# Kernel tuning notes

Hardware: AMD Instinct MI355X
Metric: run time of the kernel (lower is better)

## Reference

```python
import jax, jax.numpy as jnp
import numpy as np

B, S, D = 8, 1024, 256
H = 8            # num_heads
HD = D // H      # head_dim
FF = 1024        # expert hidden_dim
E = 8            # num_experts
K = 2            # top-k
L = 2            # num_layers
OUT = 1000       # output_dim
EPS = 1e-5


def setup_inputs() -> dict:
    key = jax.random.key(0)
    ks = jax.random.split(key, 20)
    std = 0.02
    inp = {
        "x": jax.random.normal(ks[0], (B, S, D), jnp.float32),
        "qkv_w": jax.random.normal(ks[1], (L, D, 3 * D), jnp.float32) * std,
        "qkv_b": jnp.zeros((L, 3 * D), jnp.float32),
        "attn_w": jax.random.normal(ks[2], (L, D, D), jnp.float32) * std,
        "attn_b": jnp.zeros((L, D), jnp.float32),
        "gate_w": jax.random.normal(ks[3], (L, D, E), jnp.float32) * std,
        "gate_b": jnp.zeros((L, E), jnp.float32),
        "e_w1": jax.random.normal(ks[4], (L, E, D, FF), jnp.float32) * std,
        "e_b1": jnp.zeros((L, E, FF), jnp.float32),
        "e_w2": jax.random.normal(ks[5], (L, E, FF, D), jnp.float32) * std,
        "e_b2": jnp.zeros((L, E, D), jnp.float32),
        "ln1_g": jnp.ones((D,), jnp.float32),
        "ln1_b": jnp.zeros((D,), jnp.float32),
        "ln2_g": jnp.ones((D,), jnp.float32),
        "ln2_b": jnp.zeros((D,), jnp.float32),
        "head_w": jax.random.normal(ks[6], (D, OUT), jnp.float32) * std,
        "head_b": jnp.zeros((OUT,), jnp.float32),
    }
    return inp


def _layer_norm(x, g, b):
    m = jnp.mean(x, -1, keepdims=True)
    v = jnp.mean((x - m) ** 2, -1, keepdims=True)
    return (x - m) / jnp.sqrt(v + EPS) * g + b


def _attention(x, w_qkv, b_qkv, w_o, b_o):
    # x: [B,S,D]
    qkv = (x @ w_qkv + b_qkv).reshape(B, S, 3, H, HD)
    q, k, v = jnp.moveaxis(qkv, 2, 0)            # each [B,S,H,HD]
    q = q.transpose(0, 2, 1, 3)                   # [B,H,S,HD]
    k = k.transpose(0, 2, 1, 3)
    v = v.transpose(0, 2, 1, 3)
    attn = jax.nn.softmax(jnp.einsum('bhqd,bhkd->bhqk', q, k) * (HD ** -0.5), axis=-1)
    o = jnp.einsum('bhqk,bhkd->bhqd', attn, v).transpose(0, 2, 1, 3).reshape(B, S, D)
    return o @ w_o + b_o


def _moe(x, gw, gb, w1, b1, w2, b2):
    # x: [B,S,D] -> tokens [T,D]
    xf = x.reshape(-1, D)
    gates = xf @ gw + gb                           # [T,E]
    scores, idx = jax.lax.top_k(gates, K)          # [T,K]
    gate_w = jax.nn.softmax(scores, axis=-1)       # [T,K]
    # dense all-expert compute, then gather selected experts per token
    h = jax.nn.gelu(jnp.einsum('td,edh->teh', xf, w1) + b1, approximate=False)
    eo = jnp.einsum('teh,ehd->ted', h, w2) + b2    # [T,E,D]
    sel = jnp.take_along_axis(eo, idx[:, :, None], axis=1)  # [T,K,D]
    out = jnp.sum(gate_w[:, :, None] * sel, axis=1)
    return out.reshape(B, S, D)


def reference(x, qkv_w, qkv_b, attn_w, attn_b, gate_w, gate_b,
              e_w1, e_b1, e_w2, e_b2, ln1_g, ln1_b, ln2_g, ln2_b,
              head_w, head_b):
    for l in range(L):
        x = x + _attention(_layer_norm(x, ln1_g, ln1_b),
                           qkv_w[l], qkv_b[l], attn_w[l], attn_b[l])
        x = x + _moe(_layer_norm(x, ln2_g, ln2_b),
                     gate_w[l], gate_b[l], e_w1[l], e_b1[l], e_w2[l], e_b2[l])
    pooled = jnp.mean(x, axis=1)                   # [B,D]
    return pooled @ head_w + head_b                # [B,OUT]
```

## Files before the change

kernel.cpp:

```cpp
#include <hip/hip_runtime.h>
#include <math.h>

#define TOK   8192
#define DIM   256
#define NH    8
#define HDIM  32
#define FFD   1024
#define NE    8
#define NL    2
#define NOUT  1000
#define NSLOT 16384

typedef unsigned int uint;
typedef unsigned short ushort;
typedef __attribute__((ext_vector_type(8))) short short8;
typedef __attribute__((ext_vector_type(4))) float f32x4;

#define WS_X     ((size_t)0)
#define WS_LN    (WS_X    + (size_t)TOK*DIM)
#define WS_QKV   (WS_LN   + (size_t)TOK*DIM)
#define WS_H     (WS_QKV  + (size_t)TOK*3*DIM)
#define WS_SOUT  (WS_H    + (size_t)NSLOT*256)
#define WS_GV    (WS_SOUT + (size_t)NSLOT*256)
#define WS_PP    (WS_GV   + (size_t)TOK*2)
#define WS_POOL  (WS_PP   + (size_t)8*32*256)
#define WS_INT   (WS_POOL + (size_t)8*256)
#define WS_U16   (WS_INT  + (size_t)54144)
#define WS_BIG   (WS_U16  + (size_t)2359296)

#define IB_COUNTS   0
#define IB_NTILES   8
#define IB_OFFS     16
#define IB_CURS     24
#define IB_TILE_E   32
#define IB_TILE_R0  320
#define IB_TILE_RE  608
#define IB_GIDX     896
#define IB_SPOS     17280
#define IB_STOK     33664
#define IB_BLKC     50048
#define IB_BLKB     52096

__device__ __forceinline__ float gelu_exact(float v) {
    return 0.5f * v * (1.0f + erff(v * 0.70710678118654752f));
}

__device__ __forceinline__ ushort rnd_bf16(float x) {
    uint u = __float_as_uint(x);
    return (ushort)((u + 0x7FFFu + ((u >> 16) & 1u)) >> 16);
}

__device__ __forceinline__ void split2(float x, ushort& h, ushort& lo) {
    uint u = __float_as_uint(x);
    uint hh = (u + 0x7FFFu + ((u >> 16) & 1u)) >> 16;
    h = (ushort)hh;
    float hf = __uint_as_float(hh << 16);
    float l = x - hf;
    uint ul = __float_as_uint(l);
    lo = (ushort)((ul + 0x7FFFu + ((ul >> 16) & 1u)) >> 16);
}

__device__ __forceinline__ void gld16(const ushort* g, ushort* l) {
    __builtin_amdgcn_global_load_lds(
        (const __attribute__((address_space(1))) uint*)g,
        (__attribute__((address_space(3))) uint*)l, 16, 0, 0);
}

template<bool WF32>
__global__ __launch_bounds__(256) void ln_split(const float* __restrict__ x,
                                                float* __restrict__ out,
                                                ushort* __restrict__ ohi,
                                                const float* __restrict__ g,
                                                const float* __restrict__ b) {
    int wave = threadIdx.x >> 6;
    int lane = threadIdx.x & 63;
    int t = blockIdx.x * 4 + wave;
    const float* xp = x + (size_t)t * DIM;
    float4 v = *(const float4*)&xp[lane * 4];
    float s = v.x + v.y + v.z + v.w;
    #pragma unroll
    for (int off = 32; off; off >>= 1) s += __shfl_xor(s, off);
    float mean = s * (1.0f / 256.0f);
    float dx = v.x - mean, dy = v.y - mean, dz = v.z - mean, dw = v.w - mean;
    float vs = dx * dx + dy * dy + dz * dz + dw * dw;
    #pragma unroll
    for (int off = 32; off; off >>= 1) vs += __shfl_xor(vs, off);
    float inv = rsqrtf(vs * (1.0f / 256.0f) + 1e-5f);
    float4 gg = *(const float4*)&g[lane * 4];
    float4 bb = *(const float4*)&b[lane * 4];
    float o0 = dx * inv * gg.x + bb.x;
    float o1 = dy * inv * gg.y + bb.y;
    float o2 = dz * inv * gg.z + bb.z;
    float o3 = dw * inv * gg.w + bb.w;
    size_t idx = (size_t)t * DIM + lane * 4;
    if (WF32) {
        float4 o; o.x = o0; o.y = o1; o.z = o2; o.w = o3;
        *(float4*)&out[idx] = o;
    }
    uint2 ph;
    ph.x = (uint)rnd_bf16(o0) | ((uint)rnd_bf16(o1) << 16);
    ph.y = (uint)rnd_bf16(o2) | ((uint)rnd_bf16(o3) << 16);
    *(uint2*)&ohi[idx] = ph;
}

template<bool WLO>
__global__ __launch_bounds__(256) void split_transpose(const float* __restrict__ src,
                                                       ushort* __restrict__ dhi,
                                                       ushort* __restrict__ dlo,
                                                       int K, int N) {
    int z = blockIdx.z;
    const float* s = src + (size_t)z * K * N;
    ushort* th = dhi + (size_t)z * K * N;
    ushort* tl = dlo + (size_t)z * K * N;
    __shared__ float tile[32][33];
    int k0 = blockIdx.x * 32, n0 = blockIdx.y * 32;
    int tx = threadIdx.x & 31, ty = threadIdx.x >> 5;
    #pragma unroll
    for (int i = 0; i < 4; ++i) {
        int k = k0 + ty + i * 8;
        tile[ty + i * 8][tx] = s[(size_t)k * N + n0 + tx];
    }
    __syncthreads();
    #pragma unroll
    for (int i = 0; i < 4; ++i) {
        int n = n0 + ty + i * 8;
        float v = tile[tx][ty + i * 8];
        ushort h, lo;
        split2(v, h, lo);
        th[(size_t)n * K + k0 + tx] = h;
        if (WLO) tl[(size_t)n * K + k0 + tx] = lo;
    }
}


template<int MODE, int APASS>
__global__ __launch_bounds__(256) void mfma_dense128x64(const ushort* __restrict__ Ah,
                                                        const ushort* __restrict__ Al,
                                                        const ushort* __restrict__ Bh,
                                                        const ushort* __restrict__ Bl,
                                                        const float* __restrict__ bias,
                                                        float* __restrict__ C,
                                                        ushort* __restrict__ Chi, int N) {
    __shared__ ushort LAh[128][32], LBh[64][32], LBl[64][32];
    __shared__ ushort LAl[APASS == 2 ? 128 : 2][32];
    int tid = threadIdx.x;
    int w = tid >> 6, l = tid & 63, c = l & 15, G = l >> 4;
    int row0 = blockIdx.x * 128, col0 = blockIdx.y * 64;
    int lr = l >> 2, sd = l & 3;
    int rA0 = w * 16 + lr, rA1 = 64 + rA0;
    size_t ga0 = (size_t)(row0 + rA0) * 256 + ((sd ^ ((rA0 >> 1) & 3)) << 3);
    size_t ga1 = (size_t)(row0 + rA1) * 256 + ((sd ^ ((rA1 >> 1) & 3)) << 3);
    size_t gb0 = (size_t)(col0 + rA0) * 256 + ((sd ^ ((rA0 >> 1) & 3)) << 3);
    ushort* dA0h = &LAh[w * 16][0];      ushort* dA1h = &LAh[64 + w * 16][0];
    ushort* dBh  = &LBh[w * 16][0];      ushort* dBl  = &LBl[w * 16][0];
    f32x4 acc[2][4] = {};
    for (int k0 = 0; k0 < 256; k0 += 32) {
        gld16(&Ah[ga0 + k0], dA0h);
        gld16(&Ah[ga1 + k0], dA1h);
        if (APASS == 2) {
            gld16(&Al[ga0 + k0], &LAl[w * 16][0]);
            gld16(&Al[ga1 + k0], &LAl[64 + w * 16][0]);
        }
        gld16(&Bh[gb0 + k0], dBh);
        gld16(&Bl[gb0 + k0], dBl);
        __syncthreads();
        int ar = w * 32 + c;
        short8 a_h[2], a_l[2];
        #pragma unroll
        for (int i = 0; i < 2; ++i) {
            int r = ar + i * 16;
            int sg = (G ^ ((r >> 1) & 3)) << 3;
            a_h[i] = *(const short8*)&LAh[r][sg];
            if (APASS == 2) a_l[i] = *(const short8*)&LAl[r][sg];
        }
        #pragma unroll
        for (int j = 0; j < 4; ++j) {
            int r = j * 16 + c;
            int sg = (G ^ ((r >> 1) & 3)) << 3;
            short8 b_h = *(const short8*)&LBh[r][sg];
            short8 b_l = *(const short8*)&LBl[r][sg];
            #pragma unroll
            for (int i = 0; i < 2; ++i) {
                acc[i][j] = __builtin_amdgcn_mfma_f32_16x16x32_bf16(a_h[i], b_h, acc[i][j], 0, 0, 0);
                acc[i][j] = __builtin_amdgcn_mfma_f32_16x16x32_bf16(a_h[i], b_l, acc[i][j], 0, 0, 0);
                if (APASS == 2)
                    acc[i][j] = __builtin_amdgcn_mfma_f32_16x16x32_bf16(a_l[i], b_h, acc[i][j], 0, 0, 0);
            }
        }
        __syncthreads();
    }
    int rbase = row0 + w * 32 + G * 4;
    #pragma unroll
    for (int i = 0; i < 2; ++i) {
        #pragma unroll
        for (int j = 0; j < 4; ++j) {
            int gc = col0 + j * 16 + c;
            float bv = bias[gc];
            #pragma unroll
            for (int rr = 0; rr < 4; ++rr) {
                int grow = rbase + i * 16 + rr;
                size_t idx = (size_t)grow * N + gc;
                float v = acc[i][j][rr] + bv;
                if (MODE == 1) v += C[idx];
                if (MODE == 3) {
                    Chi[idx] = rnd_bf16(v);
                } else {
                    C[idx] = v;
                }
            }
        }
    }
}

__global__ __launch_bounds__(256) void vt_kernel(const ushort* __restrict__ qkvh,
                                                 ushort* __restrict__ vth) {
    int bh = blockIdx.y;
    int b = bh >> 3, h = bh & 7;
    int kv0 = blockIdx.x * 32;
    __shared__ ushort smh[32][33];
    int tid = threadIdx.x;
    #pragma unroll
    for (int p = 0; p < 4; ++p) {
        int kv = p * 8 + (tid >> 5);
        int d = tid & 31;
        size_t src = ((size_t)(b * 1024 + kv0 + kv)) * 768 + 512 + h * 32 + d;
        smh[kv][d] = qkvh[src];
    }
    __syncthreads();
    #pragma unroll
    for (int p = 0; p < 4; ++p) {
        int d = p * 8 + (tid >> 5);
        int kv = tid & 31;
        size_t dst = ((size_t)(bh * 32 + d)) * 1024 + kv0 + kv;
        vth[dst] = smh[kv][d];
    }
}

__global__ __launch_bounds__(256, 4) void attention_mfma(const ushort* __restrict__ qkvh,
                                                         const ushort* __restrict__ vth,
                                                         ushort* __restrict__ ohi) {
    int b = blockIdx.z, h = blockIdx.y;
    int q0 = blockIdx.x * 64;
    int tid = threadIdx.x;
    int w = tid >> 6, l = tid & 63;
    int c = l & 15, g = l >> 4;
    __shared__ ushort Kh[64][40];
    __shared__ ushort VTh[32][72];
    __shared__ ushort Ph[4][16][76];

    size_t qbase = ((size_t)(b * 1024 + q0 + w * 16 + c)) * 768 + h * 32 + g * 8;
    short8 qa_h = *(const short8*)&qkvh[qbase];

    f32x4 acc_o[2] = {};
    float lpart[4] = {0.f, 0.f, 0.f, 0.f};
    const float scale = 0.17677669529663687f;

    int sr = tid >> 2, sc8 = (tid & 3) * 8;
    size_t kgbase = ((size_t)(b * 1024 + sr)) * 768 + 256 + h * 32 + sc8;
    int vd = tid >> 3, vk8 = (tid & 7) * 8;
    size_t vtbase = ((size_t)((b * 8 + h) * 32 + vd)) * 1024 + vk8;

    for (int kv0 = 0; kv0 < 1024; kv0 += 64) {
        __syncthreads();
        *(uint4*)&Kh[sr][sc8]  = *(const uint4*)&qkvh[kgbase + (size_t)kv0 * 768];
        *(uint4*)&VTh[vd][vk8] = *(const uint4*)&vth[vtbase + kv0];
        __syncthreads();

        f32x4 s4[4];
        #pragma unroll
        for (int t = 0; t < 4; ++t) {
            short8 kh = *(const short8*)&Kh[t * 16 + c][g * 8];
            f32x4 a = {};
            a = __builtin_amdgcn_mfma_f32_16x16x32_bf16(qa_h, kh, a, 0, 0, 0);
            s4[t] = a;
        }

        #pragma unroll
        for (int rr = 0; rr < 4; ++rr) {
            float sum = 0.f;
            #pragma unroll
            for (int t = 0; t < 4; ++t) {
                float p = __expf(s4[t][rr] * scale);
                uint u = __float_as_uint(p);
                uint r = (u + 0x7FFFu + ((u >> 16) & 1u)) >> 16;
                Ph[w][g * 4 + rr][t * 16 + c] = (ushort)r;
                sum += __uint_as_float(r << 16);
            }
            lpart[rr] += sum;
        }
        asm volatile("s_waitcnt lgkmcnt(0)" ::: "memory");

        #pragma unroll
        for (int kt = 0; kt < 2; ++kt) {
            short8 pah = *(const short8*)&Ph[w][c][kt * 32 + g * 8];
            #pragma unroll
            for (int T = 0; T < 2; ++T) {
                short8 vh = *(const short8*)&VTh[T * 16 + c][kt * 32 + g * 8];
                acc_o[T] = __builtin_amdgcn_mfma_f32_16x16x32_bf16(pah, vh, acc_o[T], 0, 0, 0);
            }
        }
    }

    #pragma unroll
    for (int rr = 0; rr < 4; ++rr) {
        float s = lpart[rr];
        s += __shfl_xor(s, 1);
        s += __shfl_xor(s, 2);
        s += __shfl_xor(s, 4);
        s += __shfl_xor(s, 8);
        lpart[rr] = s;
    }

    #pragma unroll
    for (int rr = 0; rr < 4; ++rr) {
        float inv = 1.0f / lpart[rr];
        int q = q0 + w * 16 + g * 4 + rr;
        #pragma unroll
        for (int T = 0; T < 2; ++T) {
            float v = acc_o[T][rr] * inv;
            size_t idx = (size_t)(b * 1024 + q) * 256 + h * 32 + T * 16 + c;
            ohi[idx] = rnd_bf16(v);
        }
    }
}

__global__ __launch_bounds__(256) void mfma_ffn1_12864(const ushort* __restrict__ Ah,
                                                       const ushort* __restrict__ W1h,
                                                       const float* __restrict__ b1l,
                                                       ushort* __restrict__ hh,
                                                       const int* __restrict__ ib,
                                                       int c0, int hFF) {
    int tileIdx = blockIdx.x;
    if (tileIdx >= ib[IB_NTILES]) return;
    int e = ib[IB_TILE_E + tileIdx];
    int row0 = ib[IB_TILE_R0 + tileIdx];
    int rowend = ib[IB_TILE_RE + tileIdx];
    __shared__ ushort LAh[128][32], LBh[64][32];
    __shared__ int tok[128];
    int tid = threadIdx.x;
    if (tid < 128) {
        int sr = row0 + tid;
        tok[tid] = ib[IB_STOK + (sr < rowend ? sr : row0)];
    }
    __syncthreads();
    int w = tid >> 6, l = tid & 63, c = l & 15, G = l >> 4;
    int lr = l >> 2, sd = l & 3;
    int rA0 = w * 16 + lr, rA1 = 64 + rA0;
    int colbase = blockIdx.y * 64;
    const ushort* Bh = W1h + (size_t)e * 262144 + (size_t)(c0 + colbase) * 256;
    size_t ga0 = (size_t)tok[rA0] * 256 + ((sd ^ ((rA0 >> 1) & 3)) << 3);
    size_t ga1 = (size_t)tok[rA1] * 256 + ((sd ^ ((rA1 >> 1) & 3)) << 3);
    size_t gb0 = (size_t)rA0 * 256 + ((sd ^ ((rA0 >> 1) & 3)) << 3);
    ushort* dA0h = &LAh[w * 16][0];      ushort* dA1h = &LAh[64 + w * 16][0];
    ushort* dBh  = &LBh[w * 16][0];
    f32x4 acc[2][4] = {};
    for (int k0 = 0; k0 < 256; k0 += 32) {
        gld16(&Ah[ga0 + k0], dA0h);
        gld16(&Ah[ga1 + k0], dA1h);
        gld16(&Bh[gb0 + k0], dBh);
        __syncthreads();
        int ar = w * 32 + c;
        short8 a_h[2];
        #pragma unroll
        for (int i = 0; i < 2; ++i) {
            int r = ar + i * 16;
            int sg = (G ^ ((r >> 1) & 3)) << 3;
            a_h[i] = *(const short8*)&LAh[r][sg];
        }
        #pragma unroll
        for (int j = 0; j < 4; ++j) {
            int r = j * 16 + c;
            int sg = (G ^ ((r >> 1) & 3)) << 3;
            short8 b_h = *(const short8*)&LBh[r][sg];
            #pragma unroll
            for (int i = 0; i < 2; ++i) {
                acc[i][j] = __builtin_amdgcn_mfma_f32_16x16x32_bf16(a_h[i], b_h, acc[i][j], 0, 0, 0);
            }
        }
        __syncthreads();
    }
    int rbase = row0 + w * 32 + G * 4;
    #pragma unroll
    for (int i = 0; i < 2; ++i) {
        #pragma unroll
        for (int j = 0; j < 4; ++j) {
            int cl = colbase + j * 16 + c;
            float bv = b1l[(size_t)e * FFD + c0 + cl];
            #pragma unroll
            for (int rr = 0; rr < 4; ++rr) {
                int sr = rbase + i * 16 + rr;
                if (sr < rowend) {
                    float v = gelu_exact(acc[i][j][rr] + bv);
                    hh[(size_t)sr * hFF + cl] = rnd_bf16(v);
                }
            }
        }
    }
}

__global__ __launch_bounds__(256) void mfma_ffn2_12864(const ushort* __restrict__ Ah,
                                                       const ushort* __restrict__ W2h,
                                                       const float* __restrict__ b2l,
                                                       float* __restrict__ sout,
                                                       const int* __restrict__ ib,
                                                       int c0, int hFF) {
    int tileIdx = blockIdx.x;
    if (tileIdx >= ib[IB_NTILES]) return;
    int e = ib[IB_TILE_E + tileIdx];
    int row0 = ib[IB_TILE_R0 + tileIdx];
    int rowend = ib[IB_TILE_RE + tileIdx];
    __shared__ ushort LAh[128][32], LBh[64][32];
    int tid = threadIdx.x;
    int w = tid >> 6, l = tid & 63, c = l & 15, G = l >> 4;
    int lr = l >> 2, sd = l & 3;
    int rA0 = w * 16 + lr, rA1 = 64 + rA0;
    int colbase = blockIdx.y * 64;
    const ushort* Bh = W2h + (size_t)e * 262144;
    size_t ga0 = (size_t)(row0 + rA0) * hFF + ((sd ^ ((rA0 >> 1) & 3)) << 3);
    size_t ga1 = (size_t)(row0 + rA1) * hFF + ((sd ^ ((rA1 >> 1) & 3)) << 3);
    size_t gb0 = (size_t)(colbase + rA0) * 1024 + c0 + ((sd ^ ((rA0 >> 1) & 3)) << 3);
    ushort* dA0h = &LAh[w * 16][0];      ushort* dA1h = &LAh[64 + w * 16][0];
    ushort* dBh  = &LBh[w * 16][0];
    f32x4 acc[2][4] = {};
    for (int k0 = 0; k0 < hFF; k0 += 32) {
        gld16(&Ah[ga0 + k0], dA0h);
        gld16(&Ah[ga1 + k0], dA1h);
        gld16(&Bh[gb0 + k0], dBh);
        __syncthreads();
        int ar = w * 32 + c;
        short8 a_h[2];
        #pragma unroll
        for (int i = 0; i < 2; ++i) {
            int r = ar + i * 16;
            int sg = (G ^ ((r >> 1) & 3)) << 3;
            a_h[i] = *(const short8*)&LAh[r][sg];
        }
        #pragma unroll
        for (int j = 0; j < 4; ++j) {
            int r = j * 16 + c;
            int sg = (G ^ ((r >> 1) & 3)) << 3;
            short8 b_h = *(const short8*)&LBh[r][sg];
            #pragma unroll
            for (int i = 0; i < 2; ++i) {
                acc[i][j] = __builtin_amdgcn_mfma_f32_16x16x32_bf16(a_h[i], b_h, acc[i][j], 0, 0, 0);
            }
        }
        __syncthreads();
    }
    int rbase = row0 + w * 32 + G * 4;
    #pragma unroll
    for (int i = 0; i < 2; ++i) {
        #pragma unroll
        for (int j = 0; j < 4; ++j) {
            int n = colbase + j * 16 + c;
            float bv = b2l[(size_t)e * DIM + n];
            #pragma unroll
            for (int rr = 0; rr < 4; ++rr) {
                int sr = rbase + i * 16 + rr;
                if (sr < rowend) {
                    size_t idx = (size_t)sr * 256 + n;
                    if (c0 == 0) sout[idx] = acc[i][j][rr] + bv;
                    else         sout[idx] += acc[i][j][rr];
                }
            }
        }
    }
}

__global__ __launch_bounds__(256) void gate_topk(const float* __restrict__ lnb,
                                                 const float* __restrict__ gw,
                                                 const float* __restrict__ gb,
                                                 float* __restrict__ gv, int* __restrict__ ib) {
    __shared__ int hist[8];
    int tid = threadIdx.x;
    if (tid < 8) hist[tid] = 0;
    __syncthreads();
    int grp = tid >> 3, ln8 = tid & 7;
    int t = blockIdx.x * 32 + grp;
    const float* x = lnb + (size_t)t * DIM + ln8 * 32;
    const float* wb = gw + (size_t)ln8 * 32 * 8;
    float g[8] = {};
    #pragma unroll
    for (int d4 = 0; d4 < 8; ++d4) {
        float4 xv = *(const float4*)&x[d4 * 4];
        const float* wr = wb + d4 * 32;
        float4 wa0 = *(const float4*)&wr[0],  wb0 = *(const float4*)&wr[4];
        float4 wa1 = *(const float4*)&wr[8],  wb1 = *(const float4*)&wr[12];
        float4 wa2 = *(const float4*)&wr[16], wb2 = *(const float4*)&wr[20];
        float4 wa3 = *(const float4*)&wr[24], wb3 = *(const float4*)&wr[28];
        g[0] += xv.x * wa0.x + xv.y * wa1.x + xv.z * wa2.x + xv.w * wa3.x;
        g[1] += xv.x * wa0.y + xv.y * wa1.y + xv.z * wa2.y + xv.w * wa3.y;
        g[2] += xv.x * wa0.z + xv.y * wa1.z + xv.z * wa2.z + xv.w * wa3.z;
        g[3] += xv.x * wa0.w + xv.y * wa1.w + xv.z * wa2.w + xv.w * wa3.w;
        g[4] += xv.x * wb0.x + xv.y * wb1.x + xv.z * wb2.x + xv.w * wb3.x;
        g[5] += xv.x * wb0.y + xv.y * wb1.y + xv.z * wb2.y + xv.w * wb3.y;
        g[6] += xv.x * wb0.z + xv.y * wb1.z + xv.z * wb2.z + xv.w * wb3.z;
        g[7] += xv.x * wb0.w + xv.y * wb1.w + xv.z * wb2.w + xv.w * wb3.w;
    }
    #pragma unroll
    for (int e = 0; e < 8; ++e) {
        g[e] += __shfl_xor(g[e], 1);
        g[e] += __shfl_xor(g[e], 2);
        g[e] += __shfl_xor(g[e], 4);
    }
    if (ln8 == 0) {
        #pragma unroll
        for (int e = 0; e < 8; ++e) g[e] += gb[e];
        int i0 = 0; float s0 = g[0];
        #pragma unroll
        for (int e = 1; e < 8; ++e) if (g[e] > s0) { s0 = g[e]; i0 = e; }
        int i1 = -1; float s1 = -1e30f;
        #pragma unroll
        for (int e = 0; e < 8; ++e) if (e != i0 && g[e] > s1) { s1 = g[e]; i1 = e; }
        float e1 = __expf(s1 - s0);
        float w0v = 1.0f / (1.0f + e1);
        float w1v = e1 / (1.0f + e1);
        gv[2 * t] = w0v; gv[2 * t + 1] = w1v;
        ib[IB_GIDX + 2 * t] = i0; ib[IB_GIDX + 2 * t + 1] = i1;
        atomicAdd(&hist[i0], 1);
        atomicAdd(&hist[i1], 1);
    }
    __syncthreads();
    if (tid < 8) ib[IB_BLKC + blockIdx.x * 8 + tid] = hist[tid];
}

__global__ __launch_bounds__(256) void scan_tiles(int* ib) {
    __shared__ int bc[2048], bb[2048];
    __shared__ int counts[8], offs[8], tstart[9];
    int tid = threadIdx.x;
    for (int i = tid; i < 2048; i += 256) bc[i] = ib[IB_BLKC + i];
    __syncthreads();
    if (tid < 8) {
        int run = 0;
        for (int b = 0; b < 256; ++b) {
            bb[b * 8 + tid] = run;
            run += bc[b * 8 + tid];
        }
        counts[tid] = run;
    }
    __syncthreads();
    if (tid == 0) {
        int off = 0, ts = 0;
        for (int e = 0; e < 8; ++e) {
            offs[e] = off;
            ib[IB_OFFS + e] = off;
            tstart[e] = ts;
            ib[IB_COUNTS + e] = counts[e];
            ts += (counts[e] + 127) >> 7;
            off += counts[e];
        }
        tstart[8] = ts;
        ib[IB_NTILES] = ts;
    }
    __syncthreads();
    for (int i = tid; i < 2048; i += 256)
        ib[IB_BLKB + i] = offs[i & 7] + bb[i];
    int total = tstart[8];
    for (int idx = tid; idx < total; idx += 256) {
        int e = 0;
        while (idx >= tstart[e + 1]) ++e;
        int i = idx - tstart[e];
        ib[IB_TILE_E + idx] = e;
        ib[IB_TILE_R0 + idx] = offs[e] + i * 128;
        int rem = counts[e] - i * 128;
        ib[IB_TILE_RE + idx] = offs[e] + i * 128 + (rem < 128 ? rem : 128);
    }
}

__global__ __launch_bounds__(64) void scatter_slots(int* ib) {
    __shared__ int cnt8[8];
    int tid = threadIdx.x;
    if (tid < 8) cnt8[tid] = ib[IB_BLKB + blockIdx.x * 8 + tid];
    __syncthreads();
    int t = blockIdx.x * 32 + (tid >> 1);
    int k = tid & 1;
    int e = ib[IB_GIDX + 2 * t + k];
    int pos = atomicAdd(&cnt8[e], 1);
    ib[IB_STOK + pos] = t;
    ib[IB_SPOS + 2 * t + k] = pos;
}

__global__ __launch_bounds__(64) void moe_gather(float* __restrict__ xb,
                                                 const float* __restrict__ sout,
                                                 const float* __restrict__ gv,
                                                 const int* __restrict__ ib) {
    int t = blockIdx.x;
    int d = threadIdx.x * 4;
    int p0 = ib[IB_SPOS + 2 * t], p1 = ib[IB_SPOS + 2 * t + 1];
    float g0 = gv[2 * t], g1 = gv[2 * t + 1];
    float4 xv = *(float4*)&xb[(size_t)t * 256 + d];
    float4 s0 = *(const float4*)&sout[(size_t)p0 * 256 + d];
    float4 s1 = *(const float4*)&sout[(size_t)p1 * 256 + d];
    xv.x += g0 * s0.x + g1 * s1.x;
    xv.y += g0 * s0.y + g1 * s1.y;
    xv.z += g0 * s0.z + g1 * s1.z;
    xv.w += g0 * s0.w + g1 * s1.w;
    *(float4*)&xb[(size_t)t * 256 + d] = xv;
}

__global__ __launch_bounds__(256) void pool1(const float* __restrict__ xb, float* __restrict__ pp) {
    int b = blockIdx.x, ch = blockIdx.y, d = threadIdx.x;
    float s = 0.0f;
    for (int i = 0; i < 32; ++i) s += xb[((size_t)b * 1024 + ch * 32 + i) * 256 + d];
    pp[(size_t)(b * 32 + ch) * 256 + d] = s;
}
__global__ __launch_bounds__(256) void pool2(const float* __restrict__ pp, float* __restrict__ pool) {
    int b = blockIdx.x, d = threadIdx.x;
    float s = 0.0f;
    for (int c = 0; c < 32; ++c) s += pp[(size_t)(b * 32 + c) * 256 + d];
    pool[(size_t)b * 256 + d] = s * (1.0f / 1024.0f);
}

__global__ __launch_bounds__(256) void head_kernel(const float* __restrict__ pool,
                                                   const float* __restrict__ hw,
                                                   const float* __restrict__ hb,
                                                   float* __restrict__ out) {
    __shared__ float P[2048];
    int tid = threadIdx.x;
    for (int i = tid; i < 2048; i += 256) P[i] = pool[i];
    __syncthreads();
    int j = blockIdx.x * 256 + tid;
    if (j >= NOUT) return;
    float acc[8] = {};
    for (int d = 0; d < 256; ++d) {
        float w = hw[(size_t)d * NOUT + j];
        #pragma unroll
        for (int b = 0; b < 8; ++b) acc[b] += P[b * 256 + d] * w;
    }
    #pragma unroll
    for (int b = 0; b < 8; ++b) out[(size_t)b * NOUT + j] = acc[b] + hb[j];
}

extern "C" void kernel_launch(void* const* d_in, const int* in_sizes, int n_in,
                              void* d_out, int out_size, void* d_ws, size_t ws_size,
                              hipStream_t stream) {
    const float* x      = (const float*)d_in[0];
    const float* qkv_w  = (const float*)d_in[1];
    const float* qkv_b  = (const float*)d_in[2];
    const float* attn_w = (const float*)d_in[3];
    const float* attn_b = (const float*)d_in[4];
    const float* gate_w = (const float*)d_in[5];
    const float* gate_b = (const float*)d_in[6];
    const float* e_w1   = (const float*)d_in[7];
    const float* e_b1   = (const float*)d_in[8];
    const float* e_w2   = (const float*)d_in[9];
    const float* e_b2   = (const float*)d_in[10];
    const float* ln1_g  = (const float*)d_in[11];
    const float* ln1_b  = (const float*)d_in[12];
    const float* ln2_g  = (const float*)d_in[13];
    const float* ln2_b  = (const float*)d_in[14];
    const float* head_w = (const float*)d_in[15];
    const float* head_b = (const float*)d_in[16];
    float* out = (float*)d_out;
    float* wsf = (float*)d_ws;

    float* xb   = wsf + WS_X;
    float* lnb  = wsf + WS_LN;
    float* sob  = wsf + WS_SOUT;
    float* gv   = wsf + WS_GV;
    float* pp   = wsf + WS_PP;
    float* pool = wsf + WS_POOL;
    int*   ib   = (int*)(wsf + WS_INT);

    ushort* qkvsh = (ushort*)(wsf + WS_QKV);
    ushort* wT    = (ushort*)(wsf + WS_QKV);
    ushort* w1th  = wT;
    ushort* w2th  = wT + 4194304;
    ushort* wTdummy = wT + 6291456;

    ushort* vth = (ushort*)(wsf + WS_H);

    ushort* u16  = (ushort*)(wsf + WS_U16);
    ushort* lnh  = u16;
    ushort* qwh  = u16 + 4194304;
    ushort* qwl  = u16 + 4390912;
    ushort* awh  = u16 + 4587520;
    ushort* awl  = u16 + 4653056;

    size_t base_bytes = (size_t)WS_BIG * 4;
    int hFF = 256;
    if (ws_size >= base_bytes + (size_t)NSLOT * 1024 * 2)      hFF = 1024;
    else if (ws_size >= base_bytes + (size_t)NSLOT * 512 * 2)  hFF = 512;
    ushort* hh = (hFF == 256) ? (ushort*)(wsf + WS_H) : (ushort*)(wsf + WS_BIG);
    int NCC = 1024 / hFF;

    hipMemcpyAsync(xb, x, (size_t)TOK * DIM * sizeof(float), hipMemcpyDeviceToDevice, stream);

    for (int l = 0; l < NL; ++l) {
        ln_split<false><<<TOK / 4, 256, 0, stream>>>(xb, nullptr, lnh, ln1_g, ln1_b);
        split_transpose<true><<<dim3(8, 24, 1), 256, 0, stream>>>(
            qkv_w + (size_t)l * DIM * 3 * DIM, qwh, qwl, 256, 768);
        mfma_dense128x64<3, 1><<<dim3(64, 12), 256, 0, stream>>>(
            lnh, nullptr, qwh, qwl, qkv_b + (size_t)l * 3 * DIM, nullptr, qkvsh, 768);
        vt_kernel<<<dim3(32, 64), 256, 0, stream>>>(qkvsh, vth);
        attention_mfma<<<dim3(16, NH, 8), 256, 0, stream>>>(qkvsh, vth, lnh);
        split_transpose<true><<<dim3(8, 8, 1), 256, 0, stream>>>(
            attn_w + (size_t)l * DIM * DIM, awh, awl, 256, 256);
        mfma_dense128x64<1, 1><<<dim3(64, 4), 256, 0, stream>>>(
            lnh, nullptr, awh, awl, attn_b + (size_t)l * DIM, xb, nullptr, 256);

        ln_split<true><<<TOK / 4, 256, 0, stream>>>(xb, lnb, lnh, ln2_g, ln2_b);
        split_transpose<false><<<dim3(8, 32, 8), 256, 0, stream>>>(
            e_w1 + (size_t)l * NE * DIM * FFD, w1th, wTdummy, 256, 1024);
        split_transpose<false><<<dim3(32, 8, 8), 256, 0, stream>>>(
            e_w2 + (size_t)l * NE * FFD * DIM, w2th, wTdummy, 1024, 256);
        gate_topk<<<TOK / 32, 256, 0, stream>>>(
            lnb, gate_w + (size_t)l * DIM * NE, gate_b + (size_t)l * NE, gv, ib);
        scan_tiles<<<1, 256, 0, stream>>>(ib);
        scatter_slots<<<TOK / 32, 64, 0, stream>>>(ib);
        for (int c = 0; c < NCC; ++c) {
            mfma_ffn1_12864<<<dim3(136, hFF / 64), 256, 0, stream>>>(
                lnh, w1th, e_b1 + (size_t)l * NE * FFD, hh, ib, c * hFF, hFF);
            mfma_ffn2_12864<<<dim3(136, 4), 256, 0, stream>>>(
                hh, w2th, e_b2 + (size_t)l * NE * DIM, sob, ib, c * hFF, hFF);
        }
        moe_gather<<<TOK, 64, 0, stream>>>(xb, sob, gv, ib);
    }

    pool1<<<dim3(8, 32), 256, 0, stream>>>(xb, pp);
    pool2<<<8, 256, 0, stream>>>(pp, pool);
    head_kernel<<<4, 256, 0, stream>>>(pool, head_w, head_b, out);
}
```

Measured before the change: 360.9 us.

## Swap grid axes so column tiles share A rows, store expert outputs as bf16

The grid of the dense and expert GEMMs is transposed so that consecutive blocks walk column tiles of the same row tile, which is meant to improve L2 reuse of the A operand. When the full hidden dimension fits in workspace, the expert second GEMM writes its output in bf16 instead of fp32, halving the slot buffer traffic read by the gather kernel. The bf16 rounding of the expert outputs adds some precision loss to the residual update.

```diff
diff --git a/kernel.cpp b/kernel.cpp
--- a/kernel.cpp
+++ b/kernel.cpp
@@ -50,6 +50,10 @@
     return (ushort)((u + 0x7FFFu + ((u >> 16) & 1u)) >> 16);
 }
 
+__device__ __forceinline__ float bf16_f32(ushort h) {
+    return __uint_as_float(((uint)h) << 16);
+}
+
 __device__ __forceinline__ void split2(float x, ushort& h, ushort& lo) {
     uint u = __float_as_uint(x);
     uint hh = (u + 0x7FFFu + ((u >> 16) & 1u)) >> 16;
@@ -145,7 +149,7 @@
     __shared__ ushort LAl[APASS == 2 ? 128 : 2][32];
     int tid = threadIdx.x;
     int w = tid >> 6, l = tid & 63, c = l & 15, G = l >> 4;
-    int row0 = blockIdx.x * 128, col0 = blockIdx.y * 64;
+    int row0 = blockIdx.y * 128, col0 = blockIdx.x * 64;
     int lr = l >> 2, sd = l & 3;
     int rA0 = w * 16 + lr, rA1 = 64 + rA0;
     size_t ga0 = (size_t)(row0 + rA0) * 256 + ((sd ^ ((rA0 >> 1) & 3)) << 3);
@@ -330,7 +334,7 @@
                                                        ushort* __restrict__ hh,
                                                        const int* __restrict__ ib,
                                                        int c0, int hFF) {
-    int tileIdx = blockIdx.x;
+    int tileIdx = blockIdx.y;
     if (tileIdx >= ib[IB_NTILES]) return;
     int e = ib[IB_TILE_E + tileIdx];
     int row0 = ib[IB_TILE_R0 + tileIdx];
@@ -346,7 +350,7 @@
     int w = tid >> 6, l = tid & 63, c = l & 15, G = l >> 4;
     int lr = l >> 2, sd = l & 3;
     int rA0 = w * 16 + lr, rA1 = 64 + rA0;
-    int colbase = blockIdx.y * 64;
+    int colbase = blockIdx.x * 64;
     const ushort* Bh = W1h + (size_t)e * 262144 + (size_t)(c0 + colbase) * 256;
     size_t ga0 = (size_t)tok[rA0] * 256 + ((sd ^ ((rA0 >> 1) & 3)) << 3);
     size_t ga1 = (size_t)tok[rA1] * 256 + ((sd ^ ((rA1 >> 1) & 3)) << 3);
@@ -398,13 +402,15 @@
     }
 }
 
+template<bool OUT16>
 __global__ __launch_bounds__(256) void mfma_ffn2_12864(const ushort* __restrict__ Ah,
                                                        const ushort* __restrict__ W2h,
                                                        const float* __restrict__ b2l,
-                                                       float* __restrict__ sout,
+                                                       float* __restrict__ soutf,
+                                                       ushort* __restrict__ soutb,
                                                        const int* __restrict__ ib,
                                                        int c0, int hFF) {
-    int tileIdx = blockIdx.x;
+    int tileIdx = blockIdx.y;
     if (tileIdx >= ib[IB_NTILES]) return;
     int e = ib[IB_TILE_E + tileIdx];
     int row0 = ib[IB_TILE_R0 + tileIdx];
@@ -414,7 +420,7 @@
     int w = tid >> 6, l = tid & 63, c = l & 15, G = l >> 4;
     int lr = l >> 2, sd = l & 3;
     int rA0 = w * 16 + lr, rA1 = 64 + rA0;
-    int colbase = blockIdx.y * 64;
+    int colbase = blockIdx.x * 64;
     const ushort* Bh = W2h + (size_t)e * 262144;
     size_t ga0 = (size_t)(row0 + rA0) * hFF + ((sd ^ ((rA0 >> 1) & 3)) << 3);
     size_t ga1 = (size_t)(row0 + rA1) * hFF + ((sd ^ ((rA1 >> 1) & 3)) << 3);
@@ -459,8 +465,12 @@
                 int sr = rbase + i * 16 + rr;
                 if (sr < rowend) {
                     size_t idx = (size_t)sr * 256 + n;
-                    if (c0 == 0) sout[idx] = acc[i][j][rr] + bv;
-                    else         sout[idx] += acc[i][j][rr];
+                    if (OUT16) {
+                        soutb[idx] = rnd_bf16(acc[i][j][rr] + bv);
+                    } else {
+                        if (c0 == 0) soutf[idx] = acc[i][j][rr] + bv;
+                        else         soutf[idx] += acc[i][j][rr];
+                    }
                 }
             }
         }
@@ -580,8 +590,10 @@
     ib[IB_SPOS + 2 * t + k] = pos;
 }
 
+template<bool OUT16>
 __global__ __launch_bounds__(64) void moe_gather(float* __restrict__ xb,
-                                                 const float* __restrict__ sout,
+                                                 const float* __restrict__ soutf,
+                                                 const ushort* __restrict__ soutb,
                                                  const float* __restrict__ gv,
                                                  const int* __restrict__ ib) {
     int t = blockIdx.x;
@@ -589,12 +601,24 @@
     int p0 = ib[IB_SPOS + 2 * t], p1 = ib[IB_SPOS + 2 * t + 1];
     float g0 = gv[2 * t], g1 = gv[2 * t + 1];
     float4 xv = *(float4*)&xb[(size_t)t * 256 + d];
-    float4 s0 = *(const float4*)&sout[(size_t)p0 * 256 + d];
-    float4 s1 = *(const float4*)&sout[(size_t)p1 * 256 + d];
-    xv.x += g0 * s0.x + g1 * s1.x;
-    xv.y += g0 * s0.y + g1 * s1.y;
-    xv.z += g0 * s0.z + g1 * s1.z;
-    xv.w += g0 * s0.w + g1 * s1.w;
+    float s0x, s0y, s0z, s0w, s1x, s1y, s1z, s1w;
+    if (OUT16) {
+        uint2 a = *(const uint2*)&soutb[(size_t)p0 * 256 + d];
+        uint2 bq = *(const uint2*)&soutb[(size_t)p1 * 256 + d];
+        s0x = bf16_f32((ushort)(a.x & 0xFFFF));  s0y = bf16_f32((ushort)(a.x >> 16));
+        s0z = bf16_f32((ushort)(a.y & 0xFFFF));  s0w = bf16_f32((ushort)(a.y >> 16));
+        s1x = bf16_f32((ushort)(bq.x & 0xFFFF)); s1y = bf16_f32((ushort)(bq.x >> 16));
+        s1z = bf16_f32((ushort)(bq.y & 0xFFFF)); s1w = bf16_f32((ushort)(bq.y >> 16));
+    } else {
+        float4 a = *(const float4*)&soutf[(size_t)p0 * 256 + d];
+        float4 bq = *(const float4*)&soutf[(size_t)p1 * 256 + d];
+        s0x = a.x; s0y = a.y; s0z = a.z; s0w = a.w;
+        s1x = bq.x; s1y = bq.y; s1z = bq.z; s1w = bq.w;
+    }
+    xv.x += g0 * s0x + g1 * s1x;
+    xv.y += g0 * s0y + g1 * s1y;
+    xv.z += g0 * s0z + g1 * s1z;
+    xv.w += g0 * s0w + g1 * s1w;
     *(float4*)&xb[(size_t)t * 256 + d] = xv;
 }
 
@@ -656,7 +680,8 @@
 
     float* xb   = wsf + WS_X;
     float* lnb  = wsf + WS_LN;
-    float* sob  = wsf + WS_SOUT;
+    float* sobf = wsf + WS_SOUT;
+    ushort* sobb = (ushort*)(wsf + WS_SOUT);
     float* gv   = wsf + WS_GV;
     float* pp   = wsf + WS_PP;
     float* pool = wsf + WS_POOL;
@@ -690,13 +715,13 @@
         ln_split<false><<<TOK / 4, 256, 0, stream>>>(xb, nullptr, lnh, ln1_g, ln1_b);
         split_transpose<true><<<dim3(8, 24, 1), 256, 0, stream>>>(
             qkv_w + (size_t)l * DIM * 3 * DIM, qwh, qwl, 256, 768);
-        mfma_dense128x64<3, 1><<<dim3(64, 12), 256, 0, stream>>>(
+        mfma_dense128x64<3, 1><<<dim3(12, 64), 256, 0, stream>>>(
             lnh, nullptr, qwh, qwl, qkv_b + (size_t)l * 3 * DIM, nullptr, qkvsh, 768);
         vt_kernel<<<dim3(32, 64), 256, 0, stream>>>(qkvsh, vth);
         attention_mfma<<<dim3(16, NH, 8), 256, 0, stream>>>(qkvsh, vth, lnh);
         split_transpose<true><<<dim3(8, 8, 1), 256, 0, stream>>>(
             attn_w + (size_t)l * DIM * DIM, awh, awl, 256, 256);
-        mfma_dense128x64<1, 1><<<dim3(64, 4), 256, 0, stream>>>(
+        mfma_dense128x64<1, 1><<<dim3(4, 64), 256, 0, stream>>>(
             lnh, nullptr, awh, awl, attn_b + (size_t)l * DIM, xb, nullptr, 256);
 
         ln_split<true><<<TOK / 4, 256, 0, stream>>>(xb, lnb, lnh, ln2_g, ln2_b);
@@ -708,13 +733,21 @@
             lnb, gate_w + (size_t)l * DIM * NE, gate_b + (size_t)l * NE, gv, ib);
         scan_tiles<<<1, 256, 0, stream>>>(ib);
         scatter_slots<<<TOK / 32, 64, 0, stream>>>(ib);
-        for (int c = 0; c < NCC; ++c) {
-            mfma_ffn1_12864<<<dim3(136, hFF / 64), 256, 0, stream>>>(
-                lnh, w1th, e_b1 + (size_t)l * NE * FFD, hh, ib, c * hFF, hFF);
-            mfma_ffn2_12864<<<dim3(136, 4), 256, 0, stream>>>(
-                hh, w2th, e_b2 + (size_t)l * NE * DIM, sob, ib, c * hFF, hFF);
-        }
-        moe_gather<<<TOK, 64, 0, stream>>>(xb, sob, gv, ib);
+        if (NCC == 1) {
+            mfma_ffn1_12864<<<dim3(16, 136), 256, 0, stream>>>(
+                lnh, w1th, e_b1 + (size_t)l * NE * FFD, hh, ib, 0, 1024);
+            mfma_ffn2_12864<true><<<dim3(4, 136), 256, 0, stream>>>(
+                hh, w2th, e_b2 + (size_t)l * NE * DIM, nullptr, sobb, ib, 0, 1024);
+            moe_gather<true><<<TOK, 64, 0, stream>>>(xb, nullptr, sobb, gv, ib);
+        } else {
+            for (int c = 0; c < NCC; ++c) {
+                mfma_ffn1_12864<<<dim3(hFF / 64, 136), 256, 0, stream>>>(
+                    lnh, w1th, e_b1 + (size_t)l * NE * FFD, hh, ib, c * hFF, hFF);
+                mfma_ffn2_12864<false><<<dim3(4, 136), 256, 0, stream>>>(
+                    hh, w2th, e_b2 + (size_t)l * NE * DIM, sobf, nullptr, ib, c * hFF, hFF);
+            }
+            moe_gather<false><<<TOK, 64, 0, stream>>>(xb, sobf, nullptr, gv, ib);
+        }
     }
 
     pool1<<<dim3(8, 32), 256, 0, stream>>>(xb, pp);
```

After: 371.3 us. 1.03x slower.
